# Kernel tuning notes

Hardware: AMD Instinct MI355X
Metric: run time of the kernel (lower is better)

The kernel has to match this reference:

```python
import jax, jax.numpy as jnp
import numpy as np


def _conv(x, w, b=None):
    # x: [B,C,H,W], w: [O,I,k,k] -> [B,O,H,W] ('same' padding, stride 1)
    y = jax.lax.conv_general_dilated(
        x, w, window_strides=(1, 1), padding='SAME',
        dimension_numbers=('NCHW', 'OIHW', 'NCHW'))
    return y if b is None else y + b[None, :, None, None]


def _lstm_cell(x, h, c, wi, bi, wh, bh):
    # fused LSTM pointwise: gates = i2h(x) + h2h(h), chunks [i, f, g, o]
    gates = _conv(x, wi, bi) + _conv(h, wh, bh)
    i, f, g, o = jnp.split(gates, 4, axis=1)
    i = jax.nn.sigmoid(i)
    f = jax.nn.sigmoid(f)
    g = jnp.tanh(g)
    o = jax.nn.sigmoid(o)
    cy = f * c + i * g
    hy = o * jnp.tanh(cy)
    return hy, cy


def setup_inputs() -> dict:
    key = jax.random.key(0)
    ks = jax.random.split(key, 16)
    B, T, C, H, W = 8, 10, 64, 64, 64
    CH = 128  # hidden channels per layer
    s = 0.05  # weight scale to keep gates in the active range
    return {
        'target': jax.random.normal(ks[0], (B, T, C, H, W), jnp.float32),
        'h0': jax.random.normal(ks[1], (B, CH, H, W), jnp.float32),
        'c0': jax.random.normal(ks[2], (B, CH, H, W), jnp.float32),
        'h1': jax.random.normal(ks[3], (B, CH, H, W), jnp.float32),
        'c1': jax.random.normal(ks[4], (B, CH, H, W), jnp.float32),
        'wi0': jax.random.normal(ks[5], (4 * CH, C, 3, 3), jnp.float32) * s,
        'bi0': jax.random.normal(ks[6], (4 * CH,), jnp.float32) * s,
        'wh0': jax.random.normal(ks[7], (4 * CH, CH, 3, 3), jnp.float32) * s,
        'bh0': jax.random.normal(ks[8], (4 * CH,), jnp.float32) * s,
        'wi1': jax.random.normal(ks[9], (4 * CH, CH, 3, 3), jnp.float32) * s,
        'bi1': jax.random.normal(ks[10], (4 * CH,), jnp.float32) * s,
        'wh1': jax.random.normal(ks[11], (4 * CH, CH, 3, 3), jnp.float32) * s,
        'bh1': jax.random.normal(ks[12], (4 * CH,), jnp.float32) * s,
        'wtop': jax.random.normal(ks[13], (C, CH, 3, 3), jnp.float32) * s,
        'btop': jax.random.normal(ks[14], (C,), jnp.float32) * s,
    }


def reference(target, h0, c0, h1, c1,
              wi0, bi0, wh0, bh0,
              wi1, bi1, wh1, bh1,
              wtop, btop):
    steps = target.shape[1]
    # first output comes from the initial top-layer hidden state
    out0 = _conv(h1, wtop, btop)  # [B, C, H, W]
    # eval mode (no dropout), reverse=False, gate=False: steps 0..steps-2
    xs = jnp.moveaxis(target[:, :steps - 1], 1, 0)  # [T-1, B, C, H, W]

    def step(carry, x):
        h0_, c0_, h1_, c1_ = carry
        x1, c0n = _lstm_cell(x, h0_, c0_, wi0, bi0, wh0, bh0)
        x2, c1n = _lstm_cell(x1, h1_, c1_, wi1, bi1, wh1, bh1)
        return (x1, c0n, x2, c1n), _conv(x2, wtop, btop)

    _, outs = jax.lax.scan(step, (h0, c0, h1, c1), xs)  # [T-1, B, C, H, W]
    all_outs = jnp.concatenate([out0[None], outs], axis=0)  # [T, B, C, H, W]
    return jnp.moveaxis(all_outs, 0, 1)  # [B, T, C, H, W]
```

## Files before the change

### kernel.cpp

```cpp
#include <hip/hip_runtime.h>
#include <cstdint>
#include <cstddef>

typedef __attribute__((ext_vector_type(8))) short bf16x8;
typedef __attribute__((ext_vector_type(4))) float f32x4;

__device__ __forceinline__ unsigned short f2bf(float f) {
    union { float f; unsigned int u; } x; x.f = f;
    unsigned int u = x.u;
    unsigned int r = (u + 0x7fffu + ((u >> 16) & 1u)) >> 16;
    return (unsigned short)r;
}
__device__ __forceinline__ float sigmoidf_(float x) { return 1.0f / (1.0f + __expf(-x)); }
__device__ __forceinline__ float tanhfast_(float x) { return 2.0f / (1.0f + __expf(-2.0f * x)) - 1.0f; }

__global__ void gather_w(const float* __restrict__ wi,
                         const float* __restrict__ wh,
                         unsigned short* __restrict__ dst,
                         int CXW, int CHW, int O)
{
    int C = CXW + CHW;
    int n = O * 9 * C;
    int e = blockIdx.x * 256 + threadIdx.x;
    if (e >= n) return;
    int c = e % C;
    int r = e / C;
    int kx = r % 3; r /= 3;
    int ky = r % 3;
    int o  = r / 3;
    float v = (c < CXW)
        ? wi[((size_t)o * CXW + c) * 9 + ky * 3 + kx]
        : wh[((size_t)o * CHW + (c - CXW)) * 9 + ky * 3 + kx];
    dst[e] = f2bf(v);
}

__global__ void prep_bias(const float* __restrict__ bi0, const float* __restrict__ bh0,
                          const float* __restrict__ bi1, const float* __restrict__ bh1,
                          const float* __restrict__ btp,
                          float* __restrict__ b0, float* __restrict__ b1, float* __restrict__ btf)
{
    int i = blockIdx.x * 256 + threadIdx.x;
    if (i < 512) b0[i] = bi0[i] + bh0[i];
    else if (i < 1024) { int j = i - 512; b1[j] = bi1[j] + bh1[j]; }
    else if (i < 1088) { int j = i - 1024; btf[j] = btp[j]; }
}

template<bool F32OUT>
__global__ void tr_cl(const float* __restrict__ src,
                      void* __restrict__ dst,
                      int C, size_t src_off, size_t src_bstride,
                      size_t src_zstride, size_t dst_zstride)
{
    __shared__ float tile[128 * 65];
    const int h = blockIdx.x, b = blockIdx.y, z = blockIdx.z;
    const int tid = threadIdx.x;
    const float* s = src + src_off + (size_t)z * src_zstride + (size_t)b * src_bstride + h * 64;
    const int n = C * 64;
    for (int i = tid; i < n; i += 256) {
        int c = i >> 6, w = i & 63;
        tile[c * 65 + w] = s[(size_t)c * 4096 + w];
    }
    __syncthreads();
    for (int i = tid; i < n; i += 256) {
        int w = i / C, c = i % C;
        size_t di = (size_t)z * dst_zstride + ((size_t)((b * 64 + h) * 64 + w)) * C + c;
        float v = tile[c * 65 + w];
        if (F32OUT) ((float*)dst)[di] = v;
        else        ((unsigned short*)dst)[di] = f2bf(v);
    }
}

template<int CX, int CH>
__global__ __launch_bounds__(512, 4)
void lstm_conv(const unsigned short* __restrict__ xin,
               const unsigned short* __restrict__ hin,
               const float* __restrict__ cin,
               const unsigned short* __restrict__ wcat,
               const float* __restrict__ bias,
               unsigned short* __restrict__ hout,
               float* __restrict__ cout_)
{
    constexpr int C = CX + CH;
    constexpr int LDSW = C + 8;
    __shared__ unsigned short slab[66 * LDSW];
    constexpr int NS = (64 * C) / (8 * 512);

    const int tid = threadIdx.x;
    const int wid = tid >> 6, lane = tid & 63;
    const int quad = lane >> 4, l16 = lane & 15;
    const int ct = wid;
    const int bx = blockIdx.x;
    const int h = ((bx & 7) << 3) | (bx >> 3);
    const int b = blockIdx.y;

    f32x4 acc[4][4];
#pragma unroll
    for (int g = 0; g < 4; ++g)
#pragma unroll
        for (int nt = 0; nt < 4; ++nt)
            acc[g][nt] = (f32x4){0.f, 0.f, 0.f, 0.f};

    const unsigned short* wr[4];
#pragma unroll
    for (int g = 0; g < 4; ++g)
        wr[g] = wcat + (size_t)(g * 128 + ct * 16 + l16) * (9 * C) + quad * 8;

    int sw[NS], sc[NS], sl[NS];
#pragma unroll
    for (int s = 0; s < NS; ++s) {
        int e = (tid + s * 512) * 8;
        sw[s] = e / C; sc[s] = e % C;
        sl[s] = (sw[s] + 1) * LDSW + sc[s];
    }

    f32x4 st[NS];
    auto load_row = [&](int r) {
        if ((unsigned)r < 64u) {
            const unsigned short* xr = xin + ((size_t)b * 64 + r) * (64 * CX);
            const unsigned short* hr = hin + ((size_t)b * 64 + r) * (64 * CH);
#pragma unroll
            for (int s = 0; s < NS; ++s) {
                const unsigned short* sp = (sc[s] < CX) ? (xr + sw[s] * CX + sc[s])
                                                        : (hr + sw[s] * CH + (sc[s] - CX));
                st[s] = *(const f32x4*)sp;
            }
        } else {
#pragma unroll
            for (int s = 0; s < NS; ++s) st[s] = (f32x4){0.f, 0.f, 0.f, 0.f};
        }
    };
    auto store_row = [&]() {
#pragma unroll
        for (int s = 0; s < NS; ++s) *(f32x4*)&slab[sl[s]] = st[s];
    };

    load_row(h - 1);
    for (int e = tid; e < 2 * LDSW; e += 512)
        slab[(e < LDSW) ? e : (65 * LDSW + (e - LDSW))] = 0;
    store_row();
    __syncthreads();

#pragma unroll
    for (int ky = 0; ky < 3; ++ky) {
        if (ky < 2) load_row(h + ky);

#pragma unroll
        for (int kx = 0; kx < 3; ++kx) {
#pragma unroll
            for (int c0 = 0; c0 < C; c0 += 32) {
                bf16x8 a[4];
#pragma unroll
                for (int g = 0; g < 4; ++g)
                    a[g] = *(const bf16x8*)(wr[g] + (ky * 3 + kx) * C + c0);
#pragma unroll
                for (int nt = 0; nt < 4; ++nt) {
                    bf16x8 bb = *(const bf16x8*)&slab[(l16 + nt * 16 + kx) * LDSW + c0 + quad * 8];
#pragma unroll
                    for (int g = 0; g < 4; ++g)
                        acc[g][nt] = __builtin_amdgcn_mfma_f32_16x16x32_bf16(a[g], bb, acc[g][nt], 0, 0, 0);
                }
            }
        }

        if (ky < 2) {
            __syncthreads();
            store_row();
            __syncthreads();
        }
    }

    const int ch4 = ct * 16 + quad * 4;
    const f32x4 bi  = *(const f32x4*)&bias[0 * 128 + ch4];
    const f32x4 bfg = *(const f32x4*)&bias[1 * 128 + ch4];
    const f32x4 bg  = *(const f32x4*)&bias[2 * 128 + ch4];
    const f32x4 bo  = *(const f32x4*)&bias[3 * 128 + ch4];
#pragma unroll
    for (int nt = 0; nt < 4; ++nt) {
        const int w = l16 + nt * 16;
        const size_t base = ((size_t)((b * 64 + h) * 64 + w)) * 128 + ch4;
        f32x4 cp = *(const f32x4*)&cin[base];
        f32x4 cy;
        union { unsigned short s[4]; uint2 v; } hp;
#pragma unroll
        for (int j = 0; j < 4; ++j) {
            float ig = sigmoidf_(acc[0][nt][j] + bi[j]);
            float fg = sigmoidf_(acc[1][nt][j] + bfg[j]);
            float gg = tanhfast_(acc[2][nt][j] + bg[j]);
            float og = sigmoidf_(acc[3][nt][j] + bo[j]);
            float cyv = fg * cp[j] + ig * gg;
            cy[j] = cyv;
            hp.s[j] = f2bf(og * tanhfast_(cyv));
        }
        *(f32x4*)&cout_[base] = cy;
        *(uint2*)&hout[base] = hp.v;
    }
}

__global__ __launch_bounds__(512, 4)
void top_conv(const unsigned short* __restrict__ hin,
              const unsigned short* __restrict__ wtopc,
              const float* __restrict__ btf,
              float* __restrict__ out, int t)
{
    constexpr int C = 128;
    constexpr int LDSW = C + 8;
    __shared__ unsigned short slab[66 * LDSW];
    constexpr int NS = (64 * C) / (8 * 512);

    const int tid = threadIdx.x;
    const int wid = tid >> 6, lane = tid & 63;
    const int quad = lane >> 4, l16 = lane & 15;
    const int ct = wid & 3, nh = wid >> 2;
    const int bx = blockIdx.x;
    const int h = ((bx & 7) << 3) | (bx >> 3);
    const int b = blockIdx.y;

    f32x4 acc[2];
    acc[0] = (f32x4){0.f, 0.f, 0.f, 0.f};
    acc[1] = (f32x4){0.f, 0.f, 0.f, 0.f};

    const unsigned short* wr = wtopc + (size_t)(ct * 16 + l16) * (9 * C) + quad * 8;
    const int w0 = nh * 32 + l16;

    int sw[NS], sl[NS];
#pragma unroll
    for (int s = 0; s < NS; ++s) {
        int e = (tid + s * 512) * 8;
        sw[s] = e >> 7;
        sl[s] = (sw[s] + 1) * LDSW + (e & 127);
    }
    f32x4 st[NS];
    auto load_row = [&](int r) {
        if ((unsigned)r < 64u) {
            const unsigned short* rp = hin + ((size_t)b * 64 + r) * (64 * C);
#pragma unroll
            for (int s = 0; s < NS; ++s) st[s] = *(const f32x4*)(rp + (tid + s * 512) * 8);
        } else {
#pragma unroll
            for (int s = 0; s < NS; ++s) st[s] = (f32x4){0.f, 0.f, 0.f, 0.f};
        }
    };
    auto store_row = [&]() {
#pragma unroll
        for (int s = 0; s < NS; ++s) *(f32x4*)&slab[sl[s]] = st[s];
    };

    load_row(h - 1);
    for (int e = tid; e < 2 * LDSW; e += 512)
        slab[(e < LDSW) ? e : (65 * LDSW + (e - LDSW))] = 0;
    store_row();
    __syncthreads();

#pragma unroll
    for (int ky = 0; ky < 3; ++ky) {
        if (ky < 2) load_row(h + ky);
#pragma unroll
        for (int kx = 0; kx < 3; ++kx) {
#pragma unroll
            for (int c0 = 0; c0 < C; c0 += 32) {
                bf16x8 a = *(const bf16x8*)(wr + (ky * 3 + kx) * C + c0);
#pragma unroll
                for (int nt = 0; nt < 2; ++nt) {
                    bf16x8 bb = *(const bf16x8*)&slab[(w0 + nt * 16 + kx) * LDSW + c0 + quad * 8];
                    acc[nt] = __builtin_amdgcn_mfma_f32_16x16x32_bf16(a, bb, acc[nt], 0, 0, 0);
                }
            }
        }
        if (ky < 2) {
            __syncthreads();
            store_row();
            __syncthreads();
        }
    }

#pragma unroll
    for (int nt = 0; nt < 2; ++nt) {
        const int w = w0 + nt * 16;
#pragma unroll
        for (int j = 0; j < 4; ++j) {
            int o = ct * 16 + quad * 4 + j;
            out[(((size_t)(b * 10 + t) * 64 + o) * 64 + h) * 64 + w] = acc[nt][j] + btf[o];
        }
    }
}

extern "C" void kernel_launch(void* const* d_in, const int* in_sizes, int n_in,
                              void* d_out, int out_size, void* d_ws, size_t ws_size,
                              hipStream_t stream)
{
    const float* target = (const float*)d_in[0];
    const float* h0i = (const float*)d_in[1];
    const float* c0i = (const float*)d_in[2];
    const float* h1i = (const float*)d_in[3];
    const float* c1i = (const float*)d_in[4];
    const float* wi0 = (const float*)d_in[5];
    const float* bi0 = (const float*)d_in[6];
    const float* wh0 = (const float*)d_in[7];
    const float* bh0 = (const float*)d_in[8];
    const float* wi1 = (const float*)d_in[9];
    const float* bi1 = (const float*)d_in[10];
    const float* wh1 = (const float*)d_in[11];
    const float* bh1 = (const float*)d_in[12];
    const float* wtp = (const float*)d_in[13];
    const float* btp = (const float*)d_in[14];
    float* out = (float*)d_out;

    char* ws = (char*)d_ws;
    size_t off = 0;
    auto alloc = [&](size_t bytes) {
        char* p = ws + off;
        off += (bytes + 255) & ~(size_t)255;
        return (void*)p;
    };
    const size_t XSTEP = (size_t)8 * 64 * 64 * 64;
    unsigned short* xall  = (unsigned short*)alloc(XSTEP * 9 * 2);
    unsigned short* h0A   = (unsigned short*)alloc((size_t)8 * 64 * 64 * 128 * 2);
    unsigned short* h0B   = (unsigned short*)alloc((size_t)8 * 64 * 64 * 128 * 2);
    unsigned short* h1A   = (unsigned short*)alloc((size_t)8 * 64 * 64 * 128 * 2);
    unsigned short* h1B   = (unsigned short*)alloc((size_t)8 * 64 * 64 * 128 * 2);
    float*          c0f   = (float*)alloc((size_t)8 * 64 * 64 * 128 * 4);
    float*          c1f   = (float*)alloc((size_t)8 * 64 * 64 * 128 * 4);
    unsigned short* wcat0 = (unsigned short*)alloc((size_t)512 * 9 * 192 * 2);
    unsigned short* wcat1 = (unsigned short*)alloc((size_t)512 * 9 * 256 * 2);
    unsigned short* wtc   = (unsigned short*)alloc((size_t)64 * 9 * 128 * 2);
    float*          b0s   = (float*)alloc(512 * 4);
    float*          b1s   = (float*)alloc(512 * 4);
    float*          btf   = (float*)alloc(64 * 4);

    gather_w<<<(512 * 9 * 192 + 255) / 256, 256, 0, stream>>>(wi0, wh0, wcat0, 64, 128, 512);
    gather_w<<<(512 * 9 * 256 + 255) / 256, 256, 0, stream>>>(wi1, wh1, wcat1, 128, 128, 512);
    gather_w<<<(64 * 9 * 128 + 255) / 256, 256, 0, stream>>>(wtp, wtp, wtc, 128, 0, 64);
    prep_bias<<<5, 256, 0, stream>>>(bi0, bh0, bi1, bh1, btp, b0s, b1s, btf);

    tr_cl<false><<<dim3(64, 8, 1), 256, 0, stream>>>(h0i, h0A, 128, 0, (size_t)128 * 4096, 0, 0);
    tr_cl<false><<<dim3(64, 8, 1), 256, 0, stream>>>(h1i, h1A, 128, 0, (size_t)128 * 4096, 0, 0);
    tr_cl<true ><<<dim3(64, 8, 1), 256, 0, stream>>>(c0i, c0f, 128, 0, (size_t)128 * 4096, 0, 0);
    tr_cl<true ><<<dim3(64, 8, 1), 256, 0, stream>>>(c1i, c1f, 128, 0, (size_t)128 * 4096, 0, 0);
    tr_cl<false><<<dim3(64, 8, 9), 256, 0, stream>>>(target, xall, 64,
                                                     0, (size_t)10 * 64 * 4096,
                                                     (size_t)64 * 4096, XSTEP);

    top_conv<<<dim3(64, 8), 512, 0, stream>>>(h1A, wtc, btf, out, 0);

    unsigned short* h0p[2] = { h0A, h0B };
    unsigned short* h1p[2] = { h1A, h1B };
    for (int t = 0; t < 9; ++t) {
        int p = t & 1;
        lstm_conv<64, 128><<<dim3(64, 8), 512, 0, stream>>>(
            xall + (size_t)t * XSTEP, h0p[p], c0f, wcat0, b0s, h0p[1 - p], c0f);
        lstm_conv<128, 128><<<dim3(64, 8), 512, 0, stream>>>(
            h0p[1 - p], h1p[p], c1f, wcat1, b1s, h1p[1 - p], c1f);
        top_conv<<<dim3(64, 8), 512, 0, stream>>>(h1p[1 - p], wtc, btf, out, t + 1);
    }
}
```

Measured before the change: 2.780 ms.

## Stage conv input rows via direct global-to-LDS loads with double buffering and XOR swizzle

Replaces the register-staged row loads (global to VGPR, then LDS store) in the LSTM and top conv kernels with global_load_lds direct copies into a double-buffered LDS slab. The next input row is now prefetched while the MFMAs run on the current one, which removes one barrier per row. Padded LDS rows give way to an XOR swizzle applied at write time in the transpose and LSTM h outputs, so LDS reads avoid bank conflicts without padding. The LDS footprint grows, up to about 67 KB dynamic for layer 1, which may reduce occupancy. A zero buffer in global memory supplies the out-of-range rows.

```diff
diff --git a/kernel.cpp b/kernel.cpp
--- a/kernel.cpp
+++ b/kernel.cpp
@@ -13,6 +13,12 @@
 }
 __device__ __forceinline__ float sigmoidf_(float x) { return 1.0f / (1.0f + __expf(-x)); }
 __device__ __forceinline__ float tanhfast_(float x) { return 2.0f / (1.0f + __expf(-2.0f * x)) - 1.0f; }
+
+__device__ __forceinline__ void gld16(const void* g, void* l) {
+    __builtin_amdgcn_global_load_lds(
+        (const __attribute__((address_space(1))) unsigned int*)g,
+        (__attribute__((address_space(3))) unsigned int*)l, 16, 0, 0);
+}
 
 __global__ void gather_w(const float* __restrict__ wi,
                          const float* __restrict__ wh,
@@ -45,6 +51,11 @@
     else if (i < 1088) { int j = i - 1024; btf[j] = btp[j]; }
 }
 
+__global__ void zero_buf(float* __restrict__ p)
+{
+    p[blockIdx.x * 256 + threadIdx.x] = 0.f;
+}
+
 template<bool F32OUT>
 __global__ void tr_cl(const float* __restrict__ src,
                       void* __restrict__ dst,
@@ -63,10 +74,16 @@
     __syncthreads();
     for (int i = tid; i < n; i += 256) {
         int w = i / C, c = i % C;
-        size_t di = (size_t)z * dst_zstride + ((size_t)((b * 64 + h) * 64 + w)) * C + c;
         float v = tile[c * 65 + w];
-        if (F32OUT) ((float*)dst)[di] = v;
-        else        ((unsigned short*)dst)[di] = f2bf(v);
+        if (F32OUT) {
+            size_t di = (size_t)z * dst_zstride + ((size_t)((b * 64 + h) * 64 + w)) * C + c;
+            ((float*)dst)[di] = v;
+        } else {
+            size_t rb = ((size_t)z * dst_zstride + (size_t)((b * 64 + h) * 64) * C) * 2;
+            size_t bo = rb + (size_t)w * (C * 2)
+                      + (size_t)(((unsigned)(c * 2)) ^ (((unsigned)(w & 7)) << 4));
+            *(unsigned short*)((char*)dst + bo) = f2bf(v);
+        }
     }
 }
 
@@ -77,13 +94,15 @@
                const float* __restrict__ cin,
                const unsigned short* __restrict__ wcat,
                const float* __restrict__ bias,
+               const float* __restrict__ zbuf,
                unsigned short* __restrict__ hout,
                float* __restrict__ cout_)
 {
     constexpr int C = CX + CH;
-    constexpr int LDSW = C + 8;
-    __shared__ unsigned short slab[66 * LDSW];
-    constexpr int NS = (64 * C) / (8 * 512);
+    constexpr int XROW = CX * 2;
+    constexpr int HROW = CH * 2;
+    constexpr int SLABB = 66 * (XROW + HROW);
+    extern __shared__ __align__(16) char slab[];
 
     const int tid = threadIdx.x;
     const int wid = tid >> 6, lane = tid & 63;
@@ -105,44 +124,56 @@
     for (int g = 0; g < 4; ++g)
         wr[g] = wcat + (size_t)(g * 128 + ct * 16 + l16) * (9 * C) + quad * 8;
 
-    int sw[NS], sc[NS], sl[NS];
-#pragma unroll
-    for (int s = 0; s < NS; ++s) {
-        int e = (tid + s * 512) * 8;
-        sw[s] = e / C; sc[s] = e % C;
-        sl[s] = (sw[s] + 1) * LDSW + sc[s];
-    }
-
-    f32x4 st[NS];
-    auto load_row = [&](int r) {
+    const int xv[3] = { ((l16 + 7) & 7) << 4, (l16 & 7) << 4, ((l16 + 1) & 7) << 4 };
+
+    auto stage = [&](int r, int buf) {
+        const char* bsx;
+        const char* bsh;
         if ((unsigned)r < 64u) {
-            const unsigned short* xr = xin + ((size_t)b * 64 + r) * (64 * CX);
-            const unsigned short* hr = hin + ((size_t)b * 64 + r) * (64 * CH);
-#pragma unroll
-            for (int s = 0; s < NS; ++s) {
-                const unsigned short* sp = (sc[s] < CX) ? (xr + sw[s] * CX + sc[s])
-                                                        : (hr + sw[s] * CH + (sc[s] - CX));
-                st[s] = *(const f32x4*)sp;
-            }
-        } else {
-#pragma unroll
-            for (int s = 0; s < NS; ++s) st[s] = (f32x4){0.f, 0.f, 0.f, 0.f};
+            bsx = (const char*)xin + (size_t)(b * 64 + r) * (64 * XROW);
+            bsh = (const char*)hin + (size_t)(b * 64 + r) * (64 * HROW);
+        } else { bsx = (const char*)zbuf; bsh = (const char*)zbuf; }
+        char* dx = slab + buf * SLABB + XROW;
+        char* dh = slab + buf * SLABB + 66 * XROW + HROW;
+        constexpr int NXW = (64 * XROW) / 1024 / 8;
+        constexpr int NHW = (64 * HROW) / 1024 / 8;
+#pragma unroll
+        for (int k = 0; k < NXW; ++k) {
+            int off = (wid * NXW + k) * 1024;
+            gld16(bsx + off + lane * 16, dx + off);
+        }
+#pragma unroll
+        for (int k = 0; k < NHW; ++k) {
+            int off = (wid * NHW + k) * 1024;
+            gld16(bsh + off + lane * 16, dh + off);
         }
     };
-    auto store_row = [&]() {
-#pragma unroll
-        for (int s = 0; s < NS; ++s) *(f32x4*)&slab[sl[s]] = st[s];
-    };
-
-    load_row(h - 1);
-    for (int e = tid; e < 2 * LDSW; e += 512)
-        slab[(e < LDSW) ? e : (65 * LDSW + (e - LDSW))] = 0;
-    store_row();
+
+    {
+        constexpr int PW = (2 * (XROW + HROW)) / 4;
+        for (int i = tid; i < 2 * PW; i += 512) {
+            int bu = (i >= PW) ? 1 : 0;
+            int j = (i - bu * PW) * 4;
+            char* base = slab + bu * SLABB;
+            char* p;
+            if (j < XROW)                      p = base + j;
+            else if (j < 2 * XROW)             p = base + 65 * XROW + (j - XROW);
+            else if (j < 2 * XROW + HROW)      p = base + 66 * XROW + (j - 2 * XROW);
+            else                               p = base + 66 * XROW + 65 * HROW + (j - 2 * XROW - HROW);
+            *(unsigned int*)p = 0u;
+        }
+    }
+    stage(h - 1, 0);
+    asm volatile("s_waitcnt vmcnt(0)" ::: "memory");
     __syncthreads();
 
 #pragma unroll
     for (int ky = 0; ky < 3; ++ky) {
-        if (ky < 2) load_row(h + ky);
+        if (ky == 0) stage(h, 1);
+        else if (ky == 1) stage(h + 1, 0);
+
+        const char* sx = slab + ((ky == 1) ? SLABB : 0);
+        const char* sh = sx + 66 * XROW;
 
 #pragma unroll
         for (int kx = 0; kx < 3; ++kx) {
@@ -152,9 +183,16 @@
 #pragma unroll
                 for (int g = 0; g < 4; ++g)
                     a[g] = *(const bf16x8*)(wr[g] + (ky * 3 + kx) * C + c0);
+                constexpr bool dummy = true; (void)dummy;
+                const bool isx = (c0 < CX);
+                const char* sb = isx ? sx : sh;
+                const int ROW = isx ? XROW : HROW;
+                const int cc2 = (isx ? c0 : (c0 - CX)) * 2;
 #pragma unroll
                 for (int nt = 0; nt < 4; ++nt) {
-                    bf16x8 bb = *(const bf16x8*)&slab[(l16 + nt * 16 + kx) * LDSW + c0 + quad * 8];
+                    const char* bp = sb + (l16 + nt * 16 + kx) * ROW
+                                   + ((cc2 + quad * 16) ^ xv[kx]);
+                    bf16x8 bb = *(const bf16x8*)bp;
 #pragma unroll
                     for (int g = 0; g < 4; ++g)
                         acc[g][nt] = __builtin_amdgcn_mfma_f32_16x16x32_bf16(a[g], bb, acc[g][nt], 0, 0, 0);
@@ -163,13 +201,13 @@
         }
 
         if (ky < 2) {
+            asm volatile("s_waitcnt vmcnt(0)" ::: "memory");
             __syncthreads();
-            store_row();
-            __syncthreads();
         }
     }
 
     const int ch4 = ct * 16 + quad * 4;
+    const unsigned hoff = ((unsigned)(ch4 * 2)) ^ (((unsigned)(l16 & 7)) << 4);
     const f32x4 bi  = *(const f32x4*)&bias[0 * 128 + ch4];
     const f32x4 bfg = *(const f32x4*)&bias[1 * 128 + ch4];
     const f32x4 bg  = *(const f32x4*)&bias[2 * 128 + ch4];
@@ -177,8 +215,8 @@
 #pragma unroll
     for (int nt = 0; nt < 4; ++nt) {
         const int w = l16 + nt * 16;
-        const size_t base = ((size_t)((b * 64 + h) * 64 + w)) * 128 + ch4;
-        f32x4 cp = *(const f32x4*)&cin[base];
+        const size_t cbase = ((size_t)((b * 64 + h) * 64 + w)) * 128 + ch4;
+        f32x4 cp = *(const f32x4*)&cin[cbase];
         f32x4 cy;
         union { unsigned short s[4]; uint2 v; } hp;
 #pragma unroll
@@ -191,8 +229,9 @@
             cy[j] = cyv;
             hp.s[j] = f2bf(og * tanhfast_(cyv));
         }
-        *(f32x4*)&cout_[base] = cy;
-        *(uint2*)&hout[base] = hp.v;
+        *(f32x4*)&cout_[cbase] = cy;
+        *(uint2*)((char*)hout + (size_t)(b * 64 + h) * (size_t)(64 * 256)
+                  + (size_t)w * 256 + hoff) = hp.v;
     }
 }
 
@@ -200,12 +239,13 @@
 void top_conv(const unsigned short* __restrict__ hin,
               const unsigned short* __restrict__ wtopc,
               const float* __restrict__ btf,
+              const float* __restrict__ zbuf,
               float* __restrict__ out, int t)
 {
     constexpr int C = 128;
-    constexpr int LDSW = C + 8;
-    __shared__ unsigned short slab[66 * LDSW];
-    constexpr int NS = (64 * C) / (8 * 512);
+    constexpr int HROW = C * 2;
+    constexpr int SLABB = 66 * HROW;
+    __shared__ __align__(16) char slab[2 * SLABB];
 
     const int tid = threadIdx.x;
     const int wid = tid >> 6, lane = tid & 63;
@@ -221,39 +261,39 @@
 
     const unsigned short* wr = wtopc + (size_t)(ct * 16 + l16) * (9 * C) + quad * 8;
     const int w0 = nh * 32 + l16;
-
-    int sw[NS], sl[NS];
-#pragma unroll
-    for (int s = 0; s < NS; ++s) {
-        int e = (tid + s * 512) * 8;
-        sw[s] = e >> 7;
-        sl[s] = (sw[s] + 1) * LDSW + (e & 127);
-    }
-    f32x4 st[NS];
-    auto load_row = [&](int r) {
-        if ((unsigned)r < 64u) {
-            const unsigned short* rp = hin + ((size_t)b * 64 + r) * (64 * C);
-#pragma unroll
-            for (int s = 0; s < NS; ++s) st[s] = *(const f32x4*)(rp + (tid + s * 512) * 8);
-        } else {
-#pragma unroll
-            for (int s = 0; s < NS; ++s) st[s] = (f32x4){0.f, 0.f, 0.f, 0.f};
+    const int xv[3] = { ((l16 + 7) & 7) << 4, (l16 & 7) << 4, ((l16 + 1) & 7) << 4 };
+
+    auto stage = [&](int r, int buf) {
+        const char* bsh = ((unsigned)r < 64u)
+            ? (const char*)hin + (size_t)(b * 64 + r) * (64 * HROW)
+            : (const char*)zbuf;
+        char* dh = slab + buf * SLABB + HROW;
+#pragma unroll
+        for (int k = 0; k < 2; ++k) {
+            int off = (wid * 2 + k) * 1024;
+            gld16(bsh + off + lane * 16, dh + off);
         }
     };
-    auto store_row = [&]() {
-#pragma unroll
-        for (int s = 0; s < NS; ++s) *(f32x4*)&slab[sl[s]] = st[s];
-    };
-
-    load_row(h - 1);
-    for (int e = tid; e < 2 * LDSW; e += 512)
-        slab[(e < LDSW) ? e : (65 * LDSW + (e - LDSW))] = 0;
-    store_row();
+
+    {
+        constexpr int PW = (2 * HROW) / 4;
+        for (int i = tid; i < 2 * PW; i += 512) {
+            int bu = (i >= PW) ? 1 : 0;
+            int j = (i - bu * PW) * 4;
+            char* base = slab + bu * SLABB;
+            char* p = (j < HROW) ? (base + j) : (base + 65 * HROW + (j - HROW));
+            *(unsigned int*)p = 0u;
+        }
+    }
+    stage(h - 1, 0);
+    asm volatile("s_waitcnt vmcnt(0)" ::: "memory");
     __syncthreads();
 
 #pragma unroll
     for (int ky = 0; ky < 3; ++ky) {
-        if (ky < 2) load_row(h + ky);
+        if (ky == 0) stage(h, 1);
+        else if (ky == 1) stage(h + 1, 0);
+        const char* sh = slab + ((ky == 1) ? SLABB : 0);
 #pragma unroll
         for (int kx = 0; kx < 3; ++kx) {
 #pragma unroll
@@ -261,14 +301,15 @@
                 bf16x8 a = *(const bf16x8*)(wr + (ky * 3 + kx) * C + c0);
 #pragma unroll
                 for (int nt = 0; nt < 2; ++nt) {
-                    bf16x8 bb = *(const bf16x8*)&slab[(w0 + nt * 16 + kx) * LDSW + c0 + quad * 8];
+                    const char* bp = sh + (w0 + nt * 16 + kx) * HROW
+                                   + ((c0 * 2 + quad * 16) ^ xv[kx]);
+                    bf16x8 bb = *(const bf16x8*)bp;
                     acc[nt] = __builtin_amdgcn_mfma_f32_16x16x32_bf16(a, bb, acc[nt], 0, 0, 0);
                 }
             }
         }
         if (ky < 2) {
-            __syncthreads();
-            store_row();
+            asm volatile("s_waitcnt vmcnt(0)" ::: "memory");
             __syncthreads();
         }
     }
@@ -326,11 +367,20 @@
     float*          b0s   = (float*)alloc(512 * 4);
     float*          b1s   = (float*)alloc(512 * 4);
     float*          btf   = (float*)alloc(64 * 4);
+    float*          zpg   = (float*)alloc(16384);
+
+    constexpr int LDS_L0 = 2 * 66 * ((64 + 128) * 2);
+    constexpr int LDS_L1 = 2 * 66 * ((128 + 128) * 2);
+    hipFuncSetAttribute(reinterpret_cast<const void*>(lstm_conv<64, 128>),
+                        hipFuncAttributeMaxDynamicSharedMemorySize, LDS_L0);
+    hipFuncSetAttribute(reinterpret_cast<const void*>(lstm_conv<128, 128>),
+                        hipFuncAttributeMaxDynamicSharedMemorySize, LDS_L1);
 
     gather_w<<<(512 * 9 * 192 + 255) / 256, 256, 0, stream>>>(wi0, wh0, wcat0, 64, 128, 512);
     gather_w<<<(512 * 9 * 256 + 255) / 256, 256, 0, stream>>>(wi1, wh1, wcat1, 128, 128, 512);
     gather_w<<<(64 * 9 * 128 + 255) / 256, 256, 0, stream>>>(wtp, wtp, wtc, 128, 0, 64);
     prep_bias<<<5, 256, 0, stream>>>(bi0, bh0, bi1, bh1, btp, b0s, b1s, btf);
+    zero_buf<<<16, 256, 0, stream>>>(zpg);
 
     tr_cl<false><<<dim3(64, 8, 1), 256, 0, stream>>>(h0i, h0A, 128, 0, (size_t)128 * 4096, 0, 0);
     tr_cl<false><<<dim3(64, 8, 1), 256, 0, stream>>>(h1i, h1A, 128, 0, (size_t)128 * 4096, 0, 0);
@@ -340,16 +390,16 @@
                                                      0, (size_t)10 * 64 * 4096,
                                                      (size_t)64 * 4096, XSTEP);
 
-    top_conv<<<dim3(64, 8), 512, 0, stream>>>(h1A, wtc, btf, out, 0);
+    top_conv<<<dim3(64, 8), 512, 0, stream>>>(h1A, wtc, btf, zpg, out, 0);
 
     unsigned short* h0p[2] = { h0A, h0B };
     unsigned short* h1p[2] = { h1A, h1B };
     for (int t = 0; t < 9; ++t) {
         int p = t & 1;
-        lstm_conv<64, 128><<<dim3(64, 8), 512, 0, stream>>>(
-            xall + (size_t)t * XSTEP, h0p[p], c0f, wcat0, b0s, h0p[1 - p], c0f);
-        lstm_conv<128, 128><<<dim3(64, 8), 512, 0, stream>>>(
-            h0p[1 - p], h1p[p], c1f, wcat1, b1s, h1p[1 - p], c1f);
-        top_conv<<<dim3(64, 8), 512, 0, stream>>>(h1p[1 - p], wtc, btf, out, t + 1);
-    }
-}
+        lstm_conv<64, 128><<<dim3(64, 8), 512, LDS_L0, stream>>>(
+            xall + (size_t)t * XSTEP, h0p[p], c0f, wcat0, b0s, zpg, h0p[1 - p], c0f);
+        lstm_conv<128, 128><<<dim3(64, 8), 512, LDS_L1, stream>>>(
+            h0p[1 - p], h1p[p], c1f, wcat1, b1s, zpg, h1p[1 - p], c1f);
+        top_conv<<<dim3(64, 8), 512, 0, stream>>>(h1p[1 - p], wtc, btf, zpg, out, t + 1);
+    }
+}
```

Result: slower. 2.943 ms (+5.9%).
